# Optimization experiments

Measured on AMD Instinct MI355X. Metric: run time of the kernel, lower is better.

The kernel has to match this reference:

```python
import jax, jax.numpy as jnp
import numpy as np

B, S = 1024, 512
V, E, H, T = 50000, 300, 800, 50


def setup_inputs() -> dict:
    key = jax.random.key(0)
    ks = jax.random.split(key, 8)
    ids = jax.random.randint(ks[0], (B, S), 0, V, dtype=jnp.int64 if jax.config.jax_enable_x64 else jnp.int32)
    return {
        "ids": ids,
        "rho": jax.random.normal(ks[1], (V, E), jnp.float32) * 0.02,
        "alpha": jax.random.normal(ks[2], (T, E), jnp.float32) * 0.02,
        "W1": jax.random.normal(ks[3], (E, H), jnp.float32) * 0.05,
        "b1": jnp.zeros((H,), jnp.float32),
        "Wmu": jax.random.normal(ks[4], (H, T), jnp.float32) * 0.05,
        "bmu": jnp.zeros((T,), jnp.float32),
        "Wlv": jax.random.normal(ks[5], (H, T), jnp.float32) * 0.05,
        "blv": jnp.zeros((T,), jnp.float32),
    }


def reference(ids, rho, alpha, W1, b1, Wmu, bmu, Wlv, blv):
    b, s = ids.shape
    v = rho.shape[0]
    # bag-of-words histogram: scatter-add instead of dense one_hot+reduce_sum
    bows = jnp.zeros((b, v), rho.dtype).at[jnp.arange(b)[:, None], ids].add(1.0)
    # zero out special tokens 1 and 2 (original: x * (1 - sum(one_hot([1,2]))))
    bows = bows.at[:, jnp.array([1, 2])].set(0.0)
    normal_bows = bows / jnp.sum(bows, axis=-1, keepdims=True)
    # encoder (eval mode: dropout is identity)
    x = jnp.einsum('bv,ve->be', normal_bows, rho)
    h = jax.nn.relu(x @ W1 + b1)
    mu_theta = h @ Wmu + bmu
    logsigma_theta = h @ Wlv + blv
    kl_theta = -0.5 * jnp.sum(1.0 + logsigma_theta - mu_theta**2 - jnp.exp(logsigma_theta), axis=-1)
    # reparameterize (eval/inference mode): z = mu
    theta = jax.nn.softmax(mu_theta, axis=-1)  # [B, T]
    beta = jax.nn.softmax(jnp.einsum('te,ve->tv', alpha, rho), axis=-1)  # [T, V]
    lookup = jnp.log(theta @ beta + 1e-5)  # [B, V]
    recon_loss = -jnp.sum(lookup * bows, axis=-1)
    loss = jnp.mean(recon_loss) + jnp.mean(kl_theta)
    return theta, loss
```

## Files before the change

### kernel.cpp

```cpp
#include <hip/hip_runtime.h>
#include <math.h>


#define Bn 1024
#define Sn 512
#define Vn 50000
#define En 300
#define Hn 800
#define Tn 50
#define KP 320
#define BSTR 64
#define W1FRAG_N (50 * 10 * 64 * 8)
#define WFRAG_N  (8 * 25 * 64 * 8)

typedef __bf16 bf16x8 __attribute__((ext_vector_type(8)));
typedef float  f32x4  __attribute__((ext_vector_type(4)));

__device__ __forceinline__ float waveReduceSum(float v) {
    #pragma unroll
    for (int off = 32; off > 0; off >>= 1) v += __shfl_xor(v, off, 64);
    return v;
}
__device__ __forceinline__ float waveReduceMax(float v) {
    #pragma unroll
    for (int off = 32; off > 0; off >>= 1) v = fmaxf(v, __shfl_xor(v, off, 64));
    return v;
}
__device__ __forceinline__ unsigned short f2bf(float x) {
    unsigned u = __float_as_uint(x);
    return (unsigned short)((u + 0x7FFFu + ((u >> 16) & 1u)) >> 16);
}
__device__ __forceinline__ float bf_lo(unsigned u) { return __uint_as_float(u << 16); }
__device__ __forceinline__ float bf_hi(unsigned u) { return __uint_as_float(u & 0xFFFF0000u); }

__global__ __launch_bounds__(256) void k0_init(
        const float* __restrict__ alpha, unsigned short* __restrict__ bfrag,
        float* __restrict__ topicsum, float* __restrict__ loss,
        float* __restrict__ xbar) {
    const int gid = blockIdx.x * 256 + threadIdx.x;
    if (blockIdx.x == 0) {
        if (threadIdx.x < Tn) topicsum[threadIdx.x] = 0.f;
        if (threadIdx.x == 63) *loss = 0.f;
    }
    if (gid < Bn * En) xbar[gid] = 0.f;
    if (gid < 4 * 10 * 64 * 8) {
        int j = gid & 7;
        int lane = (gid >> 3) & 63;
        int rest = gid >> 9;
        int kt = rest % 10, w = rest / 10;
        int t = 16 * w + (lane & 15);
        int e = kt * 32 + (lane >> 4) * 8 + j;
        bfrag[gid] = (t < Tn && e < En) ? f2bf(alpha[t * En + e]) : (unsigned short)0;
    }
}

__global__ __launch_bounds__(256) void kp_prep(
        const float* __restrict__ W1, const float* __restrict__ Wmu,
        const float* __restrict__ Wlv, unsigned short* __restrict__ w1frag,
        unsigned short* __restrict__ wfrag) {
    const int gid = blockIdx.x * 256 + threadIdx.x;
    if (gid < W1FRAG_N) {
        int j = gid & 7, lane = (gid >> 3) & 63, rest = gid >> 9;
        int kt = rest % 10, nt = rest / 10;
        int e = kt * 32 + (lane >> 4) * 8 + j;
        int hcol = nt * 16 + (lane & 15);
        w1frag[gid] = (e < En) ? f2bf(W1[e * Hn + hcol]) : (unsigned short)0;
    } else {
        int g2 = gid - W1FRAG_N;
        if (g2 < WFRAG_N) {
            int j = g2 & 7, lane = (g2 >> 3) & 63, rest = g2 >> 9;
            int kt = rest % 25, nt = rest / 25;
            int k = kt * 32 + (lane >> 4) * 8 + j;
            int t = (nt & 3) * 16 + (lane & 15);
            float val = 0.f;
            if (t < Tn) val = (nt < 4) ? Wmu[k * Tn + t] : Wlv[k * Tn + t];
            wfrag[g2] = f2bf(val);
        }
    }
}

__global__ __launch_bounds__(256) void k5_cast(
        const float4* __restrict__ rho4, ushort4* __restrict__ rhoh4) {
    const int i = blockIdx.x * 256 + threadIdx.x;
    if (i < Vn * (KP / 4)) {
        int v = i / (KP / 4), s = i - v * (KP / 4);
        ushort4 p = {0, 0, 0, 0};
        if (s < En / 4) {
            float4 r = rho4[v * (En / 4) + s];
            p.x = f2bf(r.x); p.y = f2bf(r.y); p.z = f2bf(r.z); p.w = f2bf(r.w);
        }
        rhoh4[i] = p;
    }
}

__global__ __launch_bounds__(256) void k4_beta(
        const unsigned short* __restrict__ rhoh,
        const unsigned short* __restrict__ bfrag,
        unsigned int* __restrict__ betaU32, float* __restrict__ topicsum) {
    __shared__ unsigned short trans[64 * 66];
    const int tid = threadIdx.x;
    const int wave = tid >> 6, lane = tid & 63;
    const int quad = lane >> 4, l15 = lane & 15;
    const int v0 = blockIdx.x * 64;

    bf16x8 bf[10];
    #pragma unroll
    for (int kt = 0; kt < 10; ++kt)
        bf[kt] = *(const bf16x8*)(bfrag + ((wave * 10 + kt) * 64 + lane) * 8);

    float ts = 0.f;
    #pragma unroll
    for (int mt = 0; mt < 4; ++mt) {
        const int vbase = v0 + mt * 16;
        int vrow = vbase + l15; if (vrow >= Vn) vrow = Vn - 1;
        const unsigned short* arow = rhoh + (size_t)vrow * KP + quad * 8;
        f32x4 acc = {0.f, 0.f, 0.f, 0.f};
        #pragma unroll
        for (int kt = 0; kt < 10; ++kt) {
            bf16x8 a = *(const bf16x8*)(arow + kt * 32);
            acc = __builtin_amdgcn_mfma_f32_16x16x32_bf16(a, bf[kt], acc, 0, 0, 0);
        }
        #pragma unroll
        for (int r = 0; r < 4; ++r) {
            int vv = vbase + quad * 4 + r;
            float ev = (vv < Vn) ? expf(acc[r]) : 0.f;
            ts += ev;
            trans[(mt * 16 + quad * 4 + r) * 66 + 16 * wave + l15] = f2bf(ev);
        }
    }
    ts += __shfl_xor(ts, 16, 64);
    ts += __shfl_xor(ts, 32, 64);
    const int t = 16 * wave + l15;
    if (lane < 16 && t < Tn) atomicAdd(&topicsum[t], ts);
    __syncthreads();
    unsigned int* dst = betaU32 + (size_t)v0 * 32;
    const unsigned int* tr32 = (const unsigned int*)trans;
    for (int i = tid; i < 64 * 32; i += 256)
        dst[i] = tr32[(i >> 5) * 33 + (i & 31)];
}

__global__ __launch_bounds__(256) void k1_tokens_x(
        const int* __restrict__ ids, const unsigned int* __restrict__ rhoh32,
        int* __restrict__ toks, int* __restrict__ cnt2,
        float* __restrict__ xbar) {
    __shared__ int sid[256];
    __shared__ int scount;
    const int b = blockIdx.x, half = blockIdx.y, tid = threadIdx.x;
    if (tid == 0) scount = 0;
    __syncthreads();
    int id = ids[b * Sn + half * 256 + tid];
    if (id != 1 && id != 2) {
        int p = atomicAdd(&scount, 1);
        sid[p] = id;
    }
    __syncthreads();
    const int n = scount;
    if (tid < n) toks[b * Sn + half * 256 + tid] = sid[tid];
    if (tid == 0) cnt2[b * 2 + half] = n;
    if (tid < En / 2) {
        float ax = 0.f, ay = 0.f;
        for (int s = 0; s < n; ++s) {
            unsigned u = rhoh32[sid[s] * (KP / 2) + tid];
            ax += bf_lo(u);
            ay += bf_hi(u);
        }
        atomicAdd(&xbar[b * En + 2 * tid], ax);
        atomicAdd(&xbar[b * En + 2 * tid + 1], ay);
    }
}

__global__ __launch_bounds__(256) void k2a_xcast(
        const float* __restrict__ xbar, const int* __restrict__ cnt2,
        unsigned short* __restrict__ xbh) {
    const int gid = blockIdx.x * 256 + threadIdx.x;
    if (gid < Bn * KP) {
        int b = gid / KP, e = gid - b * KP;
        unsigned short out = 0;
        if (e < En) {
            float invn = 1.0f / (float)(cnt2[2 * b] + cnt2[2 * b + 1]);
            out = f2bf(xbar[b * En + e] * invn);
        }
        xbh[gid] = out;
    }
}

__global__ __launch_bounds__(256) void k2_h(
        const unsigned short* __restrict__ xbh,
        const unsigned short* __restrict__ w1frag,
        const float* __restrict__ b1, unsigned short* __restrict__ hbh) {
    const int tid = threadIdx.x;
    const int wave = tid >> 6, lane = tid & 63;
    const int quad = lane >> 4, l15 = lane & 15;
    const int b0 = blockIdx.x * 16;
    const int nt = blockIdx.y * 4 + wave;
    if (nt >= 50) return;
    const unsigned short* arow = xbh + (size_t)(b0 + l15) * KP + quad * 8;
    f32x4 acc = {0.f, 0.f, 0.f, 0.f};
    #pragma unroll
    for (int kt = 0; kt < 10; ++kt) {
        bf16x8 a = *(const bf16x8*)(arow + kt * 32);
        bf16x8 bv = *(const bf16x8*)(w1frag + ((size_t)(nt * 10 + kt) * 64 + lane) * 8);
        acc = __builtin_amdgcn_mfma_f32_16x16x32_bf16(a, bv, acc, 0, 0, 0);
    }
    const int col = nt * 16 + l15;
    const float bias = b1[col];
    #pragma unroll
    for (int r = 0; r < 4; ++r) {
        int row = b0 + quad * 4 + r;
        hbh[(size_t)row * Hn + col] = f2bf(fmaxf(acc[r] + bias, 0.f));
    }
}

__global__ __launch_bounds__(256) void k3_theta(
        const unsigned short* __restrict__ hbh,
        const unsigned short* __restrict__ wfrag,
        const float* __restrict__ bmu, const float* __restrict__ blv,
        float* __restrict__ theta, float* __restrict__ loss) {
    __shared__ float mlds[16 * 65];
    __shared__ float llds[16 * 65];
    const int tid = threadIdx.x;
    const int wave = tid >> 6, lane = tid & 63;
    const int quad = lane >> 4, l15 = lane & 15;
    const int b0 = blockIdx.x * 16;
    const unsigned short* arow = hbh + (size_t)(b0 + l15) * Hn + quad * 8;
    f32x4 am = {0.f, 0.f, 0.f, 0.f}, al = {0.f, 0.f, 0.f, 0.f};
    #pragma unroll
    for (int kt = 0; kt < 25; ++kt) {
        bf16x8 a  = *(const bf16x8*)(arow + kt * 32);
        bf16x8 bm = *(const bf16x8*)(wfrag + ((size_t)(wave * 25 + kt) * 64 + lane) * 8);
        bf16x8 bl = *(const bf16x8*)(wfrag + ((size_t)((4 + wave) * 25 + kt) * 64 + lane) * 8);
        am = __builtin_amdgcn_mfma_f32_16x16x32_bf16(a, bm, am, 0, 0, 0);
        al = __builtin_amdgcn_mfma_f32_16x16x32_bf16(a, bl, al, 0, 0, 0);
    }
    const int t = wave * 16 + l15;
    const float bm_ = (t < Tn) ? bmu[t] : 0.f;
    const float bl_ = (t < Tn) ? blv[t] : 0.f;
    #pragma unroll
    for (int r = 0; r < 4; ++r) {
        int row = quad * 4 + r;
        mlds[row * 65 + t] = am[r] + bm_;
        llds[row * 65 + t] = al[r] + bl_;
    }
    __syncthreads();
    const int tt = (lane < Tn) ? lane : (Tn - 1);
    const bool act = (lane < Tn);
    float klacc = 0.f;
    #pragma unroll
    for (int k = 0; k < 4; ++k) {
        int row = wave * 4 + k;
        float mu = mlds[row * 65 + tt];
        float lv = llds[row * 65 + tt];
        float m = waveReduceMax(act ? mu : -1e30f);
        float ex = act ? expf(mu - m) : 0.f;
        float ssum = waveReduceSum(ex);
        if (act) theta[(b0 + row) * Tn + lane] = ex / ssum;
        klacc += waveReduceSum(act ? (1.f + lv - mu * mu - expf(lv)) : 0.f);
    }
    if (lane == 0) atomicAdd(loss, -0.5f * klacc * (1.0f / (float)Bn));
}

__global__ __launch_bounds__(256) void k6_recon(
        const int* __restrict__ toks, const int* __restrict__ cnt2,
        const float* __restrict__ theta, const float* __restrict__ topicsum,
        const unsigned short* __restrict__ betaUh, float* __restrict__ loss) {
    __shared__ float sw[Tn];
    __shared__ float swred[4];
    const int b = blockIdx.x, tid = threadIdx.x;
    if (tid < Tn) sw[tid] = theta[b * Tn + tid] / topicsum[tid];
    __syncthreads();
    float wr[Tn];
    #pragma unroll
    for (int t = 0; t < Tn; ++t) wr[t] = sw[t];
    float lsum = 0.f;
    for (int half = 0; half < 2; ++half) {
        const int n = cnt2[b * 2 + half];
        for (int i = tid; i < n; i += 256) {
            int v = toks[b * Sn + half * 256 + i];
            const uint4* q = (const uint4*)(betaUh + (size_t)v * BSTR);
            float dot = 0.f;
            #pragma unroll
            for (int k = 0; k < 6; ++k) {
                uint4 u = q[k];
                int t = 8 * k;
                dot += wr[t]     * bf_lo(u.x) + wr[t + 1] * bf_hi(u.x);
                dot += wr[t + 2] * bf_lo(u.y) + wr[t + 3] * bf_hi(u.y);
                dot += wr[t + 4] * bf_lo(u.z) + wr[t + 5] * bf_hi(u.z);
                dot += wr[t + 6] * bf_lo(u.w) + wr[t + 7] * bf_hi(u.w);
            }
            unsigned d = ((const unsigned*)q)[24];
            dot += wr[48] * bf_lo(d) + wr[49] * bf_hi(d);
            lsum += logf(dot + 1e-5f);
        }
    }
    float s = waveReduceSum(lsum);
    const int wave = tid >> 6, lane = tid & 63;
    if (lane == 0) swred[wave] = s;
    __syncthreads();
    if (tid == 0) {
        float tot = swred[0] + swred[1] + swred[2] + swred[3];
        atomicAdd(loss, -tot * (1.0f / (float)Bn));
    }
}

extern "C" void kernel_launch(void* const* d_in, const int* in_sizes, int n_in,
                              void* d_out, int out_size, void* d_ws, size_t ws_size,
                              hipStream_t stream) {
    const int*   ids   = (const int*)d_in[0];
    const float* rho   = (const float*)d_in[1];
    const float* alpha = (const float*)d_in[2];
    const float* W1    = (const float*)d_in[3];
    const float* b1    = (const float*)d_in[4];
    const float* Wmu   = (const float*)d_in[5];
    const float* bmu   = (const float*)d_in[6];
    const float* Wlv   = (const float*)d_in[7];
    const float* blv   = (const float*)d_in[8];

    float* theta = (float*)d_out;
    float* loss  = theta + Bn * Tn;

    const int k4grid = (Vn + 63) / 64;
    char* w = (char*)d_ws;
    float* topicsum = (float*)w;                w += 256;
    unsigned short* bfrag = (unsigned short*)w; w += 4 * 10 * 64 * 8 * 2;
    unsigned short* w1frag = (unsigned short*)w; w += (size_t)W1FRAG_N * 2;
    unsigned short* wfrag = (unsigned short*)w;  w += (size_t)WFRAG_N * 2;
    int*   cnt2     = (int*)w;                  w += 2 * Bn * 4;
    int*   toks     = (int*)w;                  w += Bn * Sn * 4;
    float* xbar     = (float*)w;                w += Bn * En * 4;
    unsigned short* xbh = (unsigned short*)w;   w += (size_t)Bn * KP * 2;
    unsigned short* hbh = (unsigned short*)w;   w += (size_t)Bn * Hn * 2;
    unsigned short* rhoh = (unsigned short*)w;  w += (size_t)Vn * KP * 2;
    unsigned int* betaU32 = (unsigned int*)w;   w += (size_t)k4grid * 64 * 128;

    k0_init<<<(Bn * En + 255) / 256, 256, 0, stream>>>(alpha, bfrag, topicsum, loss, xbar);
    kp_prep<<<(W1FRAG_N + WFRAG_N + 255) / 256, 256, 0, stream>>>(
        W1, Wmu, Wlv, w1frag, wfrag);
    k5_cast<<<(Vn * (KP / 4) + 255) / 256, 256, 0, stream>>>(
        (const float4*)rho, (ushort4*)rhoh);
    k4_beta<<<k4grid, 256, 0, stream>>>(rhoh, bfrag, betaU32, topicsum);
    k1_tokens_x<<<dim3(Bn, 2), 256, 0, stream>>>(ids, (const unsigned int*)rhoh, toks, cnt2, xbar);
    k2a_xcast<<<(Bn * KP + 255) / 256, 256, 0, stream>>>(xbar, cnt2, xbh);
    k2_h<<<dim3(64, 13), 256, 0, stream>>>(xbh, w1frag, b1, hbh);
    k3_theta<<<64, 256, 0, stream>>>(hbh, wfrag, bmu, blv, theta, loss);
    k6_recon<<<Bn, 256, 0, stream>>>(toks, cnt2, theta, topicsum,
                                     (const unsigned short*)betaU32, loss);
}
```

Measured before the change: 231.9 us.

## Split token gather over vocabulary ranges to raise parallelism in x accumulation

The embedding-sum kernel now launches 8 blocks per document, each scanning all 512 tokens but gathering only those whose id falls in its vocabulary slice, and atomically adding its partial into xbar. Block r==0 also writes the compacted full token list and a single count, which the recon and cast kernels now use in place of the two half-counts. The intent is more blocks and a shorter serial gather loop per block, plus some locality within each vocabulary slice. In exchange every block rereads the ids, and there are more atomic adds into xbar.

```diff
diff --git a/kernel.cpp b/kernel.cpp
--- a/kernel.cpp
+++ b/kernel.cpp
@@ -12,6 +12,8 @@
 #define BSTR 64
 #define W1FRAG_N (50 * 10 * 64 * 8)
 #define WFRAG_N  (8 * 25 * 64 * 8)
+#define NRANGE 8
+#define VRANGE (Vn / NRANGE)
 
 typedef __bf16 bf16x8 __attribute__((ext_vector_type(8)));
 typedef float  f32x4  __attribute__((ext_vector_type(4)));
@@ -141,43 +143,60 @@
 
 __global__ __launch_bounds__(256) void k1_tokens_x(
         const int* __restrict__ ids, const unsigned int* __restrict__ rhoh32,
-        int* __restrict__ toks, int* __restrict__ cnt2,
+        int* __restrict__ toks, int* __restrict__ cnt,
         float* __restrict__ xbar) {
-    __shared__ int sid[256];
-    __shared__ int scount;
-    const int b = blockIdx.x, half = blockIdx.y, tid = threadIdx.x;
-    if (tid == 0) scount = 0;
-    __syncthreads();
-    int id = ids[b * Sn + half * 256 + tid];
-    if (id != 1 && id != 2) {
-        int p = atomicAdd(&scount, 1);
-        sid[p] = id;
-    }
-    __syncthreads();
-    const int n = scount;
-    if (tid < n) toks[b * Sn + half * 256 + tid] = sid[tid];
-    if (tid == 0) cnt2[b * 2 + half] = n;
+    __shared__ int sid[Sn];
+    __shared__ int sfid[Sn];
+    __shared__ int scount, sfull;
+    const int blk = blockIdx.x;
+    const int r = blk & (NRANGE - 1), b = blk >> 3;
+    const int tid = threadIdx.x;
+    const int lo = r * VRANGE, hi = lo + VRANGE;
+    if (tid == 0) { scount = 0; sfull = 0; }
+    __syncthreads();
+    #pragma unroll
+    for (int s0 = 0; s0 < Sn; s0 += 256) {
+        int id = ids[b * Sn + s0 + tid];
+        bool val = (id != 1 && id != 2);
+        if (val && id >= lo && id < hi) {
+            int p = atomicAdd(&scount, 1);
+            sid[p] = id;
+        }
+        if (r == 0 && val) {
+            int p = atomicAdd(&sfull, 1);
+            sfid[p] = id;
+        }
+    }
+    __syncthreads();
+    if (r == 0) {
+        const int nf = sfull;
+        for (int i = tid; i < nf; i += 256) toks[b * Sn + i] = sfid[i];
+        if (tid == 0) cnt[b] = nf;
+    }
+    const int m = scount;
     if (tid < En / 2) {
         float ax = 0.f, ay = 0.f;
-        for (int s = 0; s < n; ++s) {
+        for (int s = 0; s < m; ++s) {
             unsigned u = rhoh32[sid[s] * (KP / 2) + tid];
             ax += bf_lo(u);
             ay += bf_hi(u);
         }
-        atomicAdd(&xbar[b * En + 2 * tid], ax);
-        atomicAdd(&xbar[b * En + 2 * tid + 1], ay);
+        if (m > 0) {
+            atomicAdd(&xbar[b * En + 2 * tid], ax);
+            atomicAdd(&xbar[b * En + 2 * tid + 1], ay);
+        }
     }
 }
 
 __global__ __launch_bounds__(256) void k2a_xcast(
-        const float* __restrict__ xbar, const int* __restrict__ cnt2,
+        const float* __restrict__ xbar, const int* __restrict__ cnt,
         unsigned short* __restrict__ xbh) {
     const int gid = blockIdx.x * 256 + threadIdx.x;
     if (gid < Bn * KP) {
         int b = gid / KP, e = gid - b * KP;
         unsigned short out = 0;
         if (e < En) {
-            float invn = 1.0f / (float)(cnt2[2 * b] + cnt2[2 * b + 1]);
+            float invn = 1.0f / (float)cnt[b];
             out = f2bf(xbar[b * En + e] * invn);
         }
         xbh[gid] = out;
@@ -260,7 +279,7 @@
 }
 
 __global__ __launch_bounds__(256) void k6_recon(
-        const int* __restrict__ toks, const int* __restrict__ cnt2,
+        const int* __restrict__ toks, const int* __restrict__ cnt,
         const float* __restrict__ theta, const float* __restrict__ topicsum,
         const unsigned short* __restrict__ betaUh, float* __restrict__ loss) {
     __shared__ float sw[Tn];
@@ -272,25 +291,23 @@
     #pragma unroll
     for (int t = 0; t < Tn; ++t) wr[t] = sw[t];
     float lsum = 0.f;
-    for (int half = 0; half < 2; ++half) {
-        const int n = cnt2[b * 2 + half];
-        for (int i = tid; i < n; i += 256) {
-            int v = toks[b * Sn + half * 256 + i];
-            const uint4* q = (const uint4*)(betaUh + (size_t)v * BSTR);
-            float dot = 0.f;
-            #pragma unroll
-            for (int k = 0; k < 6; ++k) {
-                uint4 u = q[k];
-                int t = 8 * k;
-                dot += wr[t]     * bf_lo(u.x) + wr[t + 1] * bf_hi(u.x);
-                dot += wr[t + 2] * bf_lo(u.y) + wr[t + 3] * bf_hi(u.y);
-                dot += wr[t + 4] * bf_lo(u.z) + wr[t + 5] * bf_hi(u.z);
-                dot += wr[t + 6] * bf_lo(u.w) + wr[t + 7] * bf_hi(u.w);
-            }
-            unsigned d = ((const unsigned*)q)[24];
-            dot += wr[48] * bf_lo(d) + wr[49] * bf_hi(d);
-            lsum += logf(dot + 1e-5f);
-        }
+    const int n = cnt[b];
+    for (int i = tid; i < n; i += 256) {
+        int v = toks[b * Sn + i];
+        const uint4* q = (const uint4*)(betaUh + (size_t)v * BSTR);
+        float dot = 0.f;
+        #pragma unroll
+        for (int k = 0; k < 6; ++k) {
+            uint4 u = q[k];
+            int t = 8 * k;
+            dot += wr[t]     * bf_lo(u.x) + wr[t + 1] * bf_hi(u.x);
+            dot += wr[t + 2] * bf_lo(u.y) + wr[t + 3] * bf_hi(u.y);
+            dot += wr[t + 4] * bf_lo(u.z) + wr[t + 5] * bf_hi(u.z);
+            dot += wr[t + 6] * bf_lo(u.w) + wr[t + 7] * bf_hi(u.w);
+        }
+        unsigned d = ((const unsigned*)q)[24];
+        dot += wr[48] * bf_lo(d) + wr[49] * bf_hi(d);
+        lsum += logf(dot + 1e-5f);
     }
     float s = waveReduceSum(lsum);
     const int wave = tid >> 6, lane = tid & 63;
@@ -324,7 +341,7 @@
     unsigned short* bfrag = (unsigned short*)w; w += 4 * 10 * 64 * 8 * 2;
     unsigned short* w1frag = (unsigned short*)w; w += (size_t)W1FRAG_N * 2;
     unsigned short* wfrag = (unsigned short*)w;  w += (size_t)WFRAG_N * 2;
-    int*   cnt2     = (int*)w;                  w += 2 * Bn * 4;
+    int*   cnt      = (int*)w;                  w += Bn * 4;
     int*   toks     = (int*)w;                  w += Bn * Sn * 4;
     float* xbar     = (float*)w;                w += Bn * En * 4;
     unsigned short* xbh = (unsigned short*)w;   w += (size_t)Bn * KP * 2;
@@ -338,10 +355,11 @@
     k5_cast<<<(Vn * (KP / 4) + 255) / 256, 256, 0, stream>>>(
         (const float4*)rho, (ushort4*)rhoh);
     k4_beta<<<k4grid, 256, 0, stream>>>(rhoh, bfrag, betaU32, topicsum);
-    k1_tokens_x<<<dim3(Bn, 2), 256, 0, stream>>>(ids, (const unsigned int*)rhoh, toks, cnt2, xbar);
-    k2a_xcast<<<(Bn * KP + 255) / 256, 256, 0, stream>>>(xbar, cnt2, xbh);
+    k1_tokens_x<<<Bn * NRANGE, 256, 0, stream>>>(ids, (const unsigned int*)rhoh,
+                                                 toks, cnt, xbar);
+    k2a_xcast<<<(Bn * KP + 255) / 256, 256, 0, stream>>>(xbar, cnt, xbh);
     k2_h<<<dim3(64, 13), 256, 0, stream>>>(xbh, w1frag, b1, hbh);
     k3_theta<<<64, 256, 0, stream>>>(hbh, wfrag, bmu, blv, theta, loss);
-    k6_recon<<<Bn, 256, 0, stream>>>(toks, cnt2, theta, topicsum,
+    k6_recon<<<Bn, 256, 0, stream>>>(toks, cnt, theta, topicsum,
                                      (const unsigned short*)betaU32, loss);
 }
```

Result: faster. 224.3 us (-3.3%).
